# Kernel optimization log

Hardware: AMD Instinct MI355X
Metric: run time of the kernel (lower is better)

## Reference

```python
import jax, jax.numpy as jnp
import numpy as np

XY_MIN, XY_MAX = -1.0, 1.0
N_BINS = 8
DIM = 16
MIN_BW = 0.001
MIN_KS = 0.001
N_TRANSFORMS = 2


def _gather_last(a, idx):
    # a: (m, dim, K*), idx: (m, dim) -> (m, dim)
    return jnp.take_along_axis(a, idx[..., None], axis=-1)[..., 0]


def _rqs_forward(x, w_u, h_u, s_u):
    """Rational quadratic spline forward + log-det-Jacobian (tfp semantics).
    x: (m, dim); w_u,h_u: (m, dim*K); s_u: (m, dim*(K-1)). Returns (y, ladJ), both (m, dim)."""
    m = x.shape[0]
    K = N_BINS
    domain = XY_MAX - XY_MIN
    c = domain - K * MIN_BW
    bw = jax.nn.softmax(w_u.reshape(m, DIM, K), axis=-1) * c + MIN_BW   # bin widths
    bh = jax.nn.softmax(h_u.reshape(m, DIM, K), axis=-1) * c + MIN_BW   # bin heights
    d_int = jax.nn.softplus(s_u.reshape(m, DIM, K - 1)) + MIN_KS        # interior knot slopes
    ones = jnp.ones((m, DIM, 1), dtype=x.dtype)
    d = jnp.concatenate([ones, d_int, ones], axis=-1)                   # (m, dim, K+1), boundary slope 1
    zero = jnp.zeros((m, DIM, 1), dtype=x.dtype)
    xk = XY_MIN + jnp.concatenate([zero, jnp.cumsum(bw, axis=-1)], axis=-1)  # (m, dim, K+1)
    yk = XY_MIN + jnp.concatenate([zero, jnp.cumsum(bh, axis=-1)], axis=-1)
    # bin search: count of interior knots <= x
    idx = jnp.clip(jnp.sum(x[..., None] >= xk[..., 1:K], axis=-1), 0, K - 1)  # (m, dim) int
    wk = _gather_last(bw, idx)
    hk = _gather_last(bh, idx)
    x0 = _gather_last(xk, idx)
    y0 = _gather_last(yk, idx)
    d0 = _gather_last(d, idx)
    d1 = _gather_last(d, idx + 1)
    sk = hk / wk
    t = (x - x0) / wk
    omt = 1.0 - t
    denom = sk + (d1 + d0 - 2.0 * sk) * t * omt
    y = y0 + hk * (sk * t * t + d0 * t * omt) / denom
    ladJ = 2.0 * jnp.log(sk) + jnp.log(d1 * t * t + 2.0 * sk * t * omt + d0 * omt * omt) - 2.0 * jnp.log(denom)
    return y, ladJ


def _shift(x, shifts, forward):
    A, B = XY_MIN, XY_MAX
    if forward:
        return jnp.mod(x + shifts - A, B - A) + A
    return jnp.mod(x - shifts - A, B - A) + A


def setup_inputs() -> dict:
    key = jax.random.key(0)
    k = jax.random.split(key, 5)
    m = 131072
    x = jax.random.uniform(k[0], (m, DIM), dtype=jnp.float32) * 2.0 - 1.0  # in [-1, 1)
    w = jax.random.normal(k[1], (N_TRANSFORMS, m, DIM * N_BINS), dtype=jnp.float32)
    h = jax.random.normal(k[2], (N_TRANSFORMS, m, DIM * N_BINS), dtype=jnp.float32)
    s = jax.random.normal(k[3], (N_TRANSFORMS, m, DIM * (N_BINS - 1)), dtype=jnp.float32)
    shifts = jax.random.uniform(k[4], (N_TRANSFORMS, m, DIM), dtype=jnp.float32)
    return {"x": x, "w": w, "h": h, "s": s, "shifts": shifts}


def reference(x, w, h, s, shifts):
    """rqs_with_periodic_shift_ forward: shift -> RQS -> unshift, per transform."""
    ladJsum = jnp.zeros_like(x)
    for i in range(N_TRANSFORMS):
        x = _shift(x, shifts[i], forward=True)
        x, ladJ = _rqs_forward(x, w[i], h[i], s[i])
        ladJsum = ladJsum + ladJ
        x = _shift(x, shifts[i], forward=False)
    return x, ladJsum
```

## Files before the change

### kernel.cpp

```cpp
#include <hip/hip_runtime.h>
#include <math.h>

#define DIMC 16
#define KB 8
#define C_SCALE 1.992f
#define MIN_BW 0.001f
#define MIN_KS 0.001f

#define LOG2E 1.44269504088896340736f
#define LN2   0.69314718055994530942f

__device__ __forceinline__ float fast_exp(float v) {
    return __builtin_amdgcn_exp2f(v * LOG2E);
}
__device__ __forceinline__ float fast_log(float v) {
    return __builtin_amdgcn_logf(v) * LN2;
}
__device__ __forceinline__ float fast_rcp(float v) {
    return __builtin_amdgcn_rcpf(v);
}

__device__ __forceinline__ float softplus_f(float v) {
    float e = fast_exp(-fabsf(v));
    return fmaxf(v, 0.0f) + fast_log(1.0f + e);
}

struct TP {
    float w[KB];
    float h[KB];
    float s[KB - 1];
    float sh;
};

__device__ __forceinline__ void load8(const float* __restrict__ p, float* dst) {
    float4 a = ((const float4*)p)[0];
    float4 b = ((const float4*)p)[1];
    dst[0] = a.x; dst[1] = a.y; dst[2] = a.z; dst[3] = a.w;
    dst[4] = b.x; dst[5] = b.y; dst[6] = b.z; dst[7] = b.w;
}

__device__ __forceinline__ float transform_step(float x, const TP& p, float& ladJsum) {
    {
        float v = x + p.sh + 1.0f;
        if (v >= 2.0f) v -= 2.0f;
        x = v - 1.0f;
    }

    float wv[KB], hv[KB];
    float mxw = p.w[0], mxh = p.h[0];
    #pragma unroll
    for (int j = 1; j < KB; ++j) { mxw = fmaxf(mxw, p.w[j]); mxh = fmaxf(mxh, p.h[j]); }
    float sw = 0.0f, sh2 = 0.0f;
    #pragma unroll
    for (int j = 0; j < KB; ++j) { wv[j] = fast_exp(p.w[j] - mxw); sw  += wv[j]; }
    #pragma unroll
    for (int j = 0; j < KB; ++j) { hv[j] = fast_exp(p.h[j] - mxh); sh2 += hv[j]; }
    float iw = C_SCALE * fast_rcp(sw);
    float ih = C_SCALE * fast_rcp(sh2);
    #pragma unroll
    for (int j = 0; j < KB; ++j) { wv[j] = wv[j] * iw + MIN_BW; hv[j] = hv[j] * ih + MIN_BW; }

    float xk = -1.0f, yk = -1.0f;
    float x0 = -1.0f, y0 = -1.0f;
    float wk = wv[0], hk = hv[0];
    float sA = p.s[0], sB = p.s[0];
    bool first = true, last = false;
    #pragma unroll
    for (int j = 1; j < KB; ++j) {
        xk += wv[j - 1];
        yk += hv[j - 1];
        bool ge = (x >= xk);
        if (j == 1)      first = !ge;
        if (j == KB - 1) last  = ge;
        x0 = ge ? xk    : x0;
        y0 = ge ? yk    : y0;
        wk = ge ? wv[j] : wk;
        hk = ge ? hv[j] : hk;
        sA = ge ? p.s[j - 1] : sA;
        sB = ge ? p.s[(j < KB - 1) ? j : KB - 2] : sB;
    }
    float d0 = first ? 1.0f : softplus_f(sA) + MIN_KS;
    float d1 = last  ? 1.0f : softplus_f(sB) + MIN_KS;

    float rwk = fast_rcp(wk);
    float sk  = hk * rwk;
    float tt  = (x - x0) * rwk;
    float omt = 1.0f - tt;
    float a2  = d1 + d0 - 2.0f * sk;
    float den = sk + a2 * tt * omt;
    float rden = fast_rcp(den);
    float y   = y0 + hk * (sk * tt * tt + d0 * tt * omt) * rden;
    float num = d1 * tt * tt + 2.0f * sk * tt * omt + d0 * omt * omt;
    float skr = sk * rden;
    ladJsum += fast_log(skr * skr * num);

    {
        float u = y - p.sh + 1.0f;
        if (u < 0.0f)  u += 2.0f;
        if (u >= 2.0f) u -= 2.0f;
        return u - 1.0f;
    }
}

__global__ __launch_bounds__(256) void spline_coupling_kernel(
    const float* __restrict__ X,
    const float* __restrict__ W,
    const float* __restrict__ H,
    const float* __restrict__ S,
    const float* __restrict__ SH,
    float* __restrict__ OUT,
    int m)
{
    const int total = m * DIMC;
    const int gid = blockIdx.x * blockDim.x + threadIdx.x;
    if (gid >= total) return;
    const int row = gid >> 4;
    const int d   = gid & 15;

    const size_t b0 = (size_t)row;
    const size_t b1 = (size_t)m + (size_t)row;

    TP p0, p1;
    float x = X[gid];
    load8(W + b0 * (DIMC * KB) + d * KB, p0.w);
    load8(H + b0 * (DIMC * KB) + d * KB, p0.h);
    load8(W + b1 * (DIMC * KB) + d * KB, p1.w);
    load8(H + b1 * (DIMC * KB) + d * KB, p1.h);
    {
        const float* s0p = S + b0 * (DIMC * (KB - 1)) + d * (KB - 1);
        const float* s1p = S + b1 * (DIMC * (KB - 1)) + d * (KB - 1);
        #pragma unroll
        for (int j = 0; j < KB - 1; ++j) { p0.s[j] = s0p[j]; p1.s[j] = s1p[j]; }
    }
    p0.sh = SH[b0 * DIMC + d];
    p1.sh = SH[b1 * DIMC + d];

    float ladJsum = 0.0f;
    x = transform_step(x, p0, ladJsum);
    x = transform_step(x, p1, ladJsum);

    OUT[gid] = x;
    OUT[(size_t)total + gid] = ladJsum;
}

extern "C" void kernel_launch(void* const* d_in, const int* in_sizes, int n_in,
                              void* d_out, int out_size, void* d_ws, size_t ws_size,
                              hipStream_t stream) {
    const int total = in_sizes[0];
    const int m = total / DIMC;
    const float* X  = (const float*)d_in[0];
    const float* W  = (const float*)d_in[1];
    const float* H  = (const float*)d_in[2];
    const float* S  = (const float*)d_in[3];
    const float* SH = (const float*)d_in[4];
    float* OUT = (float*)d_out;

    const int block = 256;
    const int grid = (total + block - 1) / block;
    spline_coupling_kernel<<<grid, block, 0, stream>>>(X, W, H, S, SH, OUT, m);
}
```

Measured before the change: 366.6 us.

## Stage per-block spline parameters into LDS via async global_load_lds with overlap

```diff
diff --git a/kernel.cpp b/kernel.cpp
--- a/kernel.cpp
+++ b/kernel.cpp
@@ -1,5 +1,6 @@
 #include <hip/hip_runtime.h>
 #include <math.h>
+#include <stdint.h>
 
 #define DIMC 16
 #define KB 8
@@ -9,6 +10,18 @@
 
 #define LOG2E 1.44269504088896340736f
 #define LN2   0.69314718055994530942f
+
+#define RPB 16
+#define NCHUNK 24
+
+#define LW   0
+#define LH   2048
+#define LS   4096
+#define LSH  5888
+#define LTOT 6144
+
+typedef const uint32_t __attribute__((address_space(1)))* gas_u32p;
+typedef uint32_t __attribute__((address_space(3)))*       las_u32p;
 
 __device__ __forceinline__ float fast_exp(float v) {
     return __builtin_amdgcn_exp2f(v * LOG2E);
@@ -31,13 +44,6 @@
     float s[KB - 1];
     float sh;
 };
-
-__device__ __forceinline__ void load8(const float* __restrict__ p, float* dst) {
-    float4 a = ((const float4*)p)[0];
-    float4 b = ((const float4*)p)[1];
-    dst[0] = a.x; dst[1] = a.y; dst[2] = a.z; dst[3] = a.w;
-    dst[4] = b.x; dst[5] = b.y; dst[6] = b.z; dst[7] = b.w;
-}
 
 __device__ __forceinline__ float transform_step(float x, const TP& p, float& ladJsum) {
     {
@@ -102,6 +108,41 @@
     }
 }
 
+__device__ __forceinline__ void stage_tiles(const float* __restrict__ Wb,
+                                            const float* __restrict__ Hb,
+                                            const float* __restrict__ Sb,
+                                            const float* __restrict__ SHb,
+                                            float* lds, int wid, int lane) {
+    #pragma unroll
+    for (int k = 0; k < NCHUNK / 4; ++k) {
+        const int c = wid + k * 4;
+        const float* src;
+        if (c < 8)       src = Wb  + c * 256;
+        else if (c < 16) src = Hb  + (c - 8) * 256;
+        else if (c < 23) src = Sb  + (c - 16) * 256;
+        else             src = SHb;
+        src += lane * 4;
+        __builtin_amdgcn_global_load_lds((gas_u32p)(const void*)src,
+                                         (las_u32p)(void*)(lds + c * 256),
+                                         16, 0, 0);
+    }
+}
+
+__device__ __forceinline__ void read_params(TP& p, const float* lds, int rl, int d) {
+    const float4* wp = (const float4*)(lds + LW + rl * 128 + d * 8);
+    const float4* hp = (const float4*)(lds + LH + rl * 128 + d * 8);
+    float4 a = wp[0], b = wp[1];
+    p.w[0]=a.x; p.w[1]=a.y; p.w[2]=a.z; p.w[3]=a.w;
+    p.w[4]=b.x; p.w[5]=b.y; p.w[6]=b.z; p.w[7]=b.w;
+    a = hp[0]; b = hp[1];
+    p.h[0]=a.x; p.h[1]=a.y; p.h[2]=a.z; p.h[3]=a.w;
+    p.h[4]=b.x; p.h[5]=b.y; p.h[6]=b.z; p.h[7]=b.w;
+    const float* sv = lds + LS + rl * 112 + d * 7;
+    #pragma unroll
+    for (int j = 0; j < KB - 1; ++j) p.s[j] = sv[j];
+    p.sh = lds[LSH + rl * 16 + d];
+}
+
 __global__ __launch_bounds__(256) void spline_coupling_kernel(
     const float* __restrict__ X,
     const float* __restrict__ W,
@@ -111,36 +152,71 @@
     float* __restrict__ OUT,
     int m)
 {
+    __shared__ float lds[LTOT];
     const int total = m * DIMC;
-    const int gid = blockIdx.x * blockDim.x + threadIdx.x;
-    if (gid >= total) return;
-    const int row = gid >> 4;
-    const int d   = gid & 15;
-
-    const size_t b0 = (size_t)row;
-    const size_t b1 = (size_t)m + (size_t)row;
-
-    TP p0, p1;
-    float x = X[gid];
-    load8(W + b0 * (DIMC * KB) + d * KB, p0.w);
-    load8(H + b0 * (DIMC * KB) + d * KB, p0.h);
-    load8(W + b1 * (DIMC * KB) + d * KB, p1.w);
-    load8(H + b1 * (DIMC * KB) + d * KB, p1.h);
-    {
-        const float* s0p = S + b0 * (DIMC * (KB - 1)) + d * (KB - 1);
-        const float* s1p = S + b1 * (DIMC * (KB - 1)) + d * (KB - 1);
-        #pragma unroll
-        for (int j = 0; j < KB - 1; ++j) { p0.s[j] = s0p[j]; p1.s[j] = s1p[j]; }
-    }
-    p0.sh = SH[b0 * DIMC + d];
-    p1.sh = SH[b1 * DIMC + d];
-
-    float ladJsum = 0.0f;
-    x = transform_step(x, p0, ladJsum);
-    x = transform_step(x, p1, ladJsum);
-
-    OUT[gid] = x;
-    OUT[(size_t)total + gid] = ladJsum;
+    const int tid  = threadIdx.x;
+    const int row0 = blockIdx.x * RPB;
+    const int rl   = tid >> 4;
+    const int d    = tid & 15;
+    const int row  = row0 + rl;
+    const int gid  = row * DIMC + d;
+    const int wid  = tid >> 6;
+    const int lane = tid & 63;
+
+    if (row0 + RPB <= m) {
+        const size_t b0 = (size_t)row0;
+        const size_t b1 = (size_t)m + (size_t)row0;
+
+        float x = X[gid];
+        float ladJ = 0.0f;
+
+        stage_tiles(W + b0 * 128, H + b0 * 128, S + b0 * 112, SH + b0 * 16,
+                    lds, wid, lane);
+        __syncthreads();
+
+        TP p0;
+        read_params(p0, lds, rl, d);
+        __syncthreads();
+
+        stage_tiles(W + b1 * 128, H + b1 * 128, S + b1 * 112, SH + b1 * 16,
+                    lds, wid, lane);
+
+        x = transform_step(x, p0, ladJ);
+
+        __syncthreads();
+
+        TP p1;
+        read_params(p1, lds, rl, d);
+        x = transform_step(x, p1, ladJ);
+
+        OUT[gid] = x;
+        OUT[(size_t)total + gid] = ladJ;
+    } else {
+        if (row < m) {
+            float x = X[gid];
+            float ladJ = 0.0f;
+            #pragma unroll
+            for (int t = 0; t < 2; ++t) {
+                const size_t base = (size_t)t * m + row;
+                TP p;
+                const float4* wp = (const float4*)(W + base * (DIMC * KB) + d * KB);
+                const float4* hp = (const float4*)(H + base * (DIMC * KB) + d * KB);
+                float4 a = wp[0], b = wp[1];
+                p.w[0]=a.x; p.w[1]=a.y; p.w[2]=a.z; p.w[3]=a.w;
+                p.w[4]=b.x; p.w[5]=b.y; p.w[6]=b.z; p.w[7]=b.w;
+                a = hp[0]; b = hp[1];
+                p.h[0]=a.x; p.h[1]=a.y; p.h[2]=a.z; p.h[3]=a.w;
+                p.h[4]=b.x; p.h[5]=b.y; p.h[6]=b.z; p.h[7]=b.w;
+                const float* sp = S + base * (DIMC * (KB - 1)) + d * (KB - 1);
+                #pragma unroll
+                for (int j = 0; j < KB - 1; ++j) p.s[j] = sp[j];
+                p.sh = SH[base * DIMC + d];
+                x = transform_step(x, p, ladJ);
+            }
+            OUT[gid] = x;
+            OUT[(size_t)total + gid] = ladJ;
+        }
+    }
 }
 
 extern "C" void kernel_launch(void* const* d_in, const int* in_sizes, int n_in,
@@ -156,6 +232,6 @@
     float* OUT = (float*)d_out;
 
     const int block = 256;
-    const int grid = (total + block - 1) / block;
+    const int grid = (m + RPB - 1) / RPB;
     spline_coupling_kernel<<<grid, block, 0, stream>>>(X, W, H, S, SH, OUT, m);
 }
```

Result: no change. 364.7 us (-0.5%).
